# Performance work log

Measured on AMD Instinct MI355X. Metric: run time of the kernel, lower is better.

## Reference

```python
import jax, jax.numpy as jnp
import numpy as np

N = 20000   # nodes
E = 320000  # edges
H = 256     # hidden size == input size (no FeatEncoder branch)


def setup_inputs() -> dict:
    key = jax.random.key(0)
    ks = jax.random.split(key, 10)
    x = jax.random.normal(ks[0], (N, H), dtype=jnp.float32)
    edge_index = jax.random.randint(ks[1], (2, E), 0, N, dtype=jnp.int32)
    s = 1.0 / np.sqrt(H)  # PyG Linear default (glorot-ish uniform)
    inp = {"x": x, "edge_index": edge_index}
    for i, name in enumerate(["W1", "W1_1", "W2", "W3"]):
        inp[name] = jax.random.uniform(ks[2 + i], (H, H), jnp.float32, -s, s)
    for name in ["b1", "b1_1", "b2", "b3"]:
        inp[name] = jnp.zeros((H,), jnp.float32)
    return inp


def gcn_norm(edge_index, num_nodes):
    # add self loops (weight 1.0), symmetric normalization D^-1/2 A D^-1/2
    row, col = edge_index[0], edge_index[1]
    loop = jnp.arange(num_nodes, dtype=row.dtype)
    row = jnp.concatenate([row, loop])
    col = jnp.concatenate([col, loop])
    w = jnp.ones(row.shape[0], dtype=jnp.float32)
    deg = jax.ops.segment_sum(w, col, num_segments=num_nodes)  # in-degree at targets
    dinv = jnp.where(deg > 0, jax.lax.rsqrt(deg), 0.0)
    norm = dinv[row] * dinv[col]  # [E+N]
    return row, col, norm


def conv(x, W, b, row, col, norm, num_nodes):
    # GCNConv: linear transform, gather-scale-scatter-add, bias
    h = x @ W                                   # [N, H]
    msg = norm[:, None] * h[row]                # [E+N, H] gather + scale
    out = jax.ops.segment_sum(msg, col, num_segments=num_nodes)  # scatter-add
    return out + b


def reference(x, edge_index, W1, b1, W1_1, b1_1, W2, b2, W3, b3):
    num_nodes = x.shape[0]
    row, col, norm = gcn_norm(edge_index, num_nodes)
    h1 = jax.nn.relu(conv(x, W1, b1, row, col, norm, num_nodes))
    h2 = jax.nn.relu(conv(h1, W1_1, b1_1, row, col, norm, num_nodes))
    out2 = conv(h2, W2, b2, row, col, norm, num_nodes)
    out3 = conv(h2, W3, b3, row, col, norm, num_nodes)
    return out2, out3
```

## Files before the change

### kernel.cpp

```cpp
#include <hip/hip_runtime.h>
#include <math.h>

#define HD 256

typedef short bf16x8 __attribute__((ext_vector_type(8)));
typedef float f32x4  __attribute__((ext_vector_type(4)));

__device__ __forceinline__ unsigned short f2bf(float f) {
    unsigned u = __builtin_bit_cast(unsigned, f);
    unsigned r = (u + 0x7fffu + ((u >> 16) & 1u)) >> 16;
    return (unsigned short)r;
}
__device__ __forceinline__ float bf2f(unsigned b) {
    return __builtin_bit_cast(float, (b & 0xffffu) << 16);
}



__global__ __launch_bounds__(256) void fillpack_kernel(const int* __restrict__ ei, int E,
                                                       int* __restrict__ cursor,
                                                       int* __restrict__ csr,
                                                       const float* __restrict__ W0,
                                                       const float* __restrict__ W1,
                                                       const float* __restrict__ W2,
                                                       const float* __restrict__ W3,
                                                       unsigned short* __restrict__ pkhi,
                                                       unsigned short* __restrict__ pklo) {
    const int Eb = (E + 255) >> 8;
    const int bid = blockIdx.x;
    if (bid < Eb) {
        int idx = bid * 256 + threadIdx.x;
        if (idx >= E) return;
        int r = ei[idx];
        int c = ei[E + idx];
        int slot = atomicAdd(&cursor[c], 1);
        if (slot < 127) csr[((size_t)c << 7) + slot] = r;
    } else {
        int gid = (bid - Eb) * 256 + threadIdx.x;
        int mat  = gid >> 13;
        int rem  = gid & 8191;
        int nc   = rem >> 9;
        int kc   = (rem >> 6) & 7;
        int lane = rem & 63;
        const float* W = (mat == 0) ? W0 : (mat == 1) ? W1 : (mat == 2) ? W2 : W3;
        int col = nc * 16 + (lane & 15);
        int kb  = kc * 32 + (lane >> 4) * 8;
        alignas(16) unsigned short h[8], l[8];
#pragma unroll
        for (int e = 0; e < 8; ++e) {
            float w = W[(size_t)(kb + e) * HD + col];
            unsigned short hb = f2bf(w);
            h[e] = hb;
            l[e] = f2bf(w - bf2f(hb));
        }
        size_t off = (size_t)mat * 65536 + ((size_t)(nc * 8 + kc) * 64 + lane) * 8;
        *(uint4*)&pkhi[off] = *(const uint4*)h;
        *(uint4*)&pklo[off] = *(const uint4*)l;
    }
}


__global__ __launch_bounds__(256) void finconv_kernel(const int* __restrict__ cursor,
                                                      int* __restrict__ csr,
                                                      const float* __restrict__ x,
                                                      unsigned short* __restrict__ T,
                                                      float* __restrict__ zpad,
                                                      float* __restrict__ tpad,
                                                      int N) {
    const int Fb = (N + 255) >> 8;
    const int Cb = (N * 32 + 255) >> 8;
    const int bid = blockIdx.x;
    if (bid < Fb) {
        int v = bid * 256 + threadIdx.x;
        if (v >= N) return;
        int c = min(cursor[v], 126);
        size_t base = (size_t)v << 7;
        csr[base + c] = v;
        int pad = (c + 8) & ~7;
        for (int s = c + 1; s < pad; ++s) csr[base + s] = N;
    } else if (bid < Fb + Cb) {
        int gid = (bid - Fb) * 256 + threadIdx.x;
        if (gid >= N * 32) return;
        int row = gid >> 5;
        int q   = gid & 31;
        float s = rsqrtf((float)(min(cursor[row], 126) + 1));
        const float4* xp = (const float4*)(x + (size_t)row * HD + q * 8);
        float4 v0 = xp[0], v1 = xp[1];
        float vals[8] = {v0.x, v0.y, v0.z, v0.w, v1.x, v1.y, v1.z, v1.w};
        alignas(16) unsigned short h[8], l[8];
#pragma unroll
        for (int e = 0; e < 8; ++e) {
            float t = vals[e] * s;
            unsigned short hb = f2bf(t);
            h[e] = hb;
            l[e] = f2bf(t - bf2f(hb));
        }
        size_t o = (size_t)row * 512 + (size_t)(q >> 2) * 64 + (q & 3) * 8;
        *(uint4*)&T[o]      = *(const uint4*)h;
        *(uint4*)&T[o + 32] = *(const uint4*)l;
    } else {
        int t = threadIdx.x;
        zpad[t] = 0.f;
        tpad[t] = 0.f;
    }
}


template<int OUTMODE>
__global__ __launch_bounds__(256) void agg_chunk_kernel(const float* __restrict__ zin,
                                                        const int* __restrict__ csr,
                                                        const int* __restrict__ cursor,
                                                        const float* __restrict__ bias,
                                                        void* __restrict__ outBuf, int N) {
    const int chunk = blockIdx.x & 7;
    const int nb    = blockIdx.x >> 3;
    const int wave  = threadIdx.x >> 6;
    const int lane  = threadIdx.x & 63;
    const int slot  = lane & 7;
    const int ni    = lane >> 3;

    int v = nb * 32 + wave * 8 + ni;
    const bool valid = v < N;
    if (!valid) v = N - 1;

    const int cnt  = min(cursor[v], 126) + 1;
    const float dv = rsqrtf((float)cnt);
    const int iters = (cnt + 7) >> 3;
    const int* cp = csr + ((size_t)v << 7);

    const float4* zp = (const float4*)zin;
    const size_t cbase = (size_t)chunk * 8 + slot;

    float a0 = 0.f, a1 = 0.f, a2 = 0.f, a3 = 0.f;
    for (int it = 0; it < iters; ++it) {
        const int* q = cp + it * 8;
        int u0 = q[0], u1 = q[1], u2 = q[2], u3 = q[3];
        int u4 = q[4], u5 = q[5], u6 = q[6], u7 = q[7];
        float4 d0 = zp[(size_t)u0 * 64 + cbase];
        float4 d1 = zp[(size_t)u1 * 64 + cbase];
        float4 d2 = zp[(size_t)u2 * 64 + cbase];
        float4 d3 = zp[(size_t)u3 * 64 + cbase];
        float4 d4 = zp[(size_t)u4 * 64 + cbase];
        float4 d5 = zp[(size_t)u5 * 64 + cbase];
        float4 d6 = zp[(size_t)u6 * 64 + cbase];
        float4 d7 = zp[(size_t)u7 * 64 + cbase];
        a0 += ((d0.x + d1.x) + (d2.x + d3.x)) + ((d4.x + d5.x) + (d6.x + d7.x));
        a1 += ((d0.y + d1.y) + (d2.y + d3.y)) + ((d4.y + d5.y) + (d6.y + d7.y));
        a2 += ((d0.z + d1.z) + (d2.z + d3.z)) + ((d4.z + d5.z) + (d6.z + d7.z));
        a3 += ((d0.w + d1.w) + (d2.w + d3.w)) + ((d4.w + d5.w) + (d6.w + d7.w));
    }
    if (!valid) return;

    float t0, t1, t2, t3;
    if (OUTMODE == 2) {
        t0 = dv * a0; t1 = dv * a1; t2 = dv * a2; t3 = dv * a3;
    } else {
        float4 bv = *(const float4*)&bias[chunk * 32 + slot * 4];
        t0 = dv * fmaxf(fmaf(dv, a0, bv.x), 0.f);
        t1 = dv * fmaxf(fmaf(dv, a1, bv.y), 0.f);
        t2 = dv * fmaxf(fmaf(dv, a2, bv.z), 0.f);
        t3 = dv * fmaxf(fmaf(dv, a3, bv.w), 0.f);
    }

    if (OUTMODE == 1) {
        ((float4*)outBuf)[(size_t)v * 64 + cbase] = make_float4(t0, t1, t2, t3);
    } else {
        unsigned short h0 = f2bf(t0), h1 = f2bf(t1), h2 = f2bf(t2), h3 = f2bf(t3);
        uint2 hw, lw;
        hw.x = h0 | ((unsigned)h1 << 16);
        hw.y = h2 | ((unsigned)h3 << 16);
        unsigned short l0 = f2bf(t0 - bf2f(h0)), l1 = f2bf(t1 - bf2f(h1));
        unsigned short l2 = f2bf(t2 - bf2f(h2)), l3 = f2bf(t3 - bf2f(h3));
        lw.x = l0 | ((unsigned)l1 << 16);
        lw.y = l2 | ((unsigned)l3 << 16);
        unsigned short* T = (unsigned short*)outBuf;
        size_t o = (size_t)v * 512 + chunk * 64 + slot * 4;
        *(uint2*)&T[o]      = hw;
        *(uint2*)&T[o + 32] = lw;
    }
}


template<int NBY>
__global__ __launch_bounds__(256, 3)
void gemm_mfma_kernel(const unsigned short* __restrict__ T,
                      const unsigned short* __restrict__ pkhi,
                      const unsigned short* __restrict__ pklo,
                      const float* __restrict__ ba,
                      const float* __restrict__ bb,
                      float* __restrict__ Ca,
                      float* __restrict__ Cb, int M, int gx) {
    __shared__ unsigned short ldsW[2][2][2048];

    const int id  = blockIdx.x;
    const int xcd = id & 7;
    const int t   = id >> 3;
    const int by  = t & (NBY - 1);
    const int g   = t / NBY;
    const int bx  = xcd + (g << 3);
    if (bx >= gx) return;

    const int tid  = threadIdx.x;
    const int lane = tid & 63;
    const int wave = tid >> 6;

    const int sel = (NBY == 8) ? (by >> 2) : 0;
    const int nc0 = ((NBY == 8) ? (by & 3) : by) * 4;
    const unsigned short* ph = pkhi + (size_t)sel * 65536;
    const unsigned short* pl = pklo + (size_t)sel * 65536;
    float*       C    = sel ? Cb : Ca;
    const float* bias = sel ? bb : ba;

    const int row0  = bx * 128 + wave * 32;
    const int rowA0 = min(row0 + (lane & 15), M - 1);
    const int rowA1 = min(row0 + 16 + (lane & 15), M - 1);
    const int kg    = lane >> 4;

    const unsigned short* aT0 = T + (size_t)rowA0 * 512 + kg * 8;
    const unsigned short* aT1 = T + (size_t)rowA1 * 512 + kg * 8;

    const int snf = tid >> 6;
    const unsigned short* sph = ph + ((size_t)(nc0 + snf) * 8) * 512 + (size_t)(tid & 63) * 8;
    const unsigned short* spl = pl + ((size_t)(nc0 + snf) * 8) * 512 + (size_t)(tid & 63) * 8;

    f32x4 acc[2][4];
#pragma unroll
    for (int f = 0; f < 2; ++f)
#pragma unroll
        for (int j = 0; j < 4; ++j) acc[f][j] = (f32x4)0.f;

    uint4 sh = *(const uint4*)(sph);
    uint4 sl = *(const uint4*)(spl);
    *(uint4*)&ldsW[0][0][tid * 8] = sh;
    *(uint4*)&ldsW[0][1][tid * 8] = sl;
    sh = *(const uint4*)(sph + 512);
    sl = *(const uint4*)(spl + 512);

    bf16x8 a0h[2], a0l[2], a1h[2], a1l[2];
    a0h[0] = *(const bf16x8*)(aT0);
    a0l[0] = *(const bf16x8*)(aT0 + 32);
    a1h[0] = *(const bf16x8*)(aT1);
    a1l[0] = *(const bf16x8*)(aT1 + 32);
    __syncthreads();

#pragma unroll
    for (int kc = 0; kc < 8; ++kc) {
        const int cur = kc & 1;
        if (kc < 7) {
            a0h[cur ^ 1] = *(const bf16x8*)(aT0 + (kc + 1) * 64);
            a0l[cur ^ 1] = *(const bf16x8*)(aT0 + (kc + 1) * 64 + 32);
            a1h[cur ^ 1] = *(const bf16x8*)(aT1 + (kc + 1) * 64);
            a1l[cur ^ 1] = *(const bf16x8*)(aT1 + (kc + 1) * 64 + 32);
        }
        bf16x8 wh[4], wl[4];
#pragma unroll
        for (int j = 0; j < 4; ++j) {
            wh[j] = *(const bf16x8*)&ldsW[cur][0][((size_t)j * 64 + lane) * 8];
            wl[j] = *(const bf16x8*)&ldsW[cur][1][((size_t)j * 64 + lane) * 8];
        }
#pragma unroll
        for (int j = 0; j < 4; ++j) {
            acc[0][j] = __builtin_amdgcn_mfma_f32_16x16x32_bf16(a0h[cur], wh[j], acc[0][j], 0, 0, 0);
            acc[0][j] = __builtin_amdgcn_mfma_f32_16x16x32_bf16(a0h[cur], wl[j], acc[0][j], 0, 0, 0);
            acc[0][j] = __builtin_amdgcn_mfma_f32_16x16x32_bf16(a0l[cur], wh[j], acc[0][j], 0, 0, 0);
            acc[1][j] = __builtin_amdgcn_mfma_f32_16x16x32_bf16(a1h[cur], wh[j], acc[1][j], 0, 0, 0);
            acc[1][j] = __builtin_amdgcn_mfma_f32_16x16x32_bf16(a1h[cur], wl[j], acc[1][j], 0, 0, 0);
            acc[1][j] = __builtin_amdgcn_mfma_f32_16x16x32_bf16(a1l[cur], wh[j], acc[1][j], 0, 0, 0);
        }
        if (kc < 7) {
            *(uint4*)&ldsW[cur ^ 1][0][tid * 8] = sh;
            *(uint4*)&ldsW[cur ^ 1][1][tid * 8] = sl;
            if (kc < 6) {
                sh = *(const uint4*)(sph + (size_t)(kc + 2) * 512);
                sl = *(const uint4*)(spl + (size_t)(kc + 2) * 512);
            }
            __syncthreads();
        }
    }

#pragma unroll
    for (int nf = 0; nf < 4; ++nf) {
        int col = (nc0 + nf) * 16 + (lane & 15);
        float badd = (NBY == 8) ? bias[col] : 0.f;
#pragma unroll
        for (int f = 0; f < 2; ++f) {
#pragma unroll
            for (int r = 0; r < 4; ++r) {
                int row = row0 + f * 16 + kg * 4 + r;
                if (row < M) C[(size_t)row * HD + col] = acc[f][nf][r] + badd;
            }
        }
    }
}


static inline size_t align_up(size_t x, size_t a) { return (x + a - 1) & ~(a - 1); }

extern "C" void kernel_launch(void* const* d_in, const int* in_sizes, int n_in,
                              void* d_out, int out_size, void* d_ws, size_t ws_size,
                              hipStream_t stream) {
    const int N = in_sizes[0] / HD;
    const int E = in_sizes[1] / 2;

    const float* x   = (const float*)d_in[0];
    const int*   ei  = (const int*)d_in[1];
    const float* W1  = (const float*)d_in[2];
    const float* W11 = (const float*)d_in[3];
    const float* W2  = (const float*)d_in[4];
    const float* W3  = (const float*)d_in[5];
    const float* b1  = (const float*)d_in[6];
    const float* b11 = (const float*)d_in[7];
    const float* b2  = (const float*)d_in[8];
    const float* b3  = (const float*)d_in[9];

    float* out2 = (float*)d_out;
    float* out3 = out2 + (size_t)N * HD;

    char* p = (char*)d_ws;
    int*   cursor = (int*)p;   p += align_up((size_t)N * 4, 256);
    int*   csr    = (int*)p;   p += align_up((size_t)N * 128 * 4, 256);
    unsigned short* pkhi = (unsigned short*)p; p += align_up((size_t)4 * 65536 * 2, 256);
    unsigned short* pklo = (unsigned short*)p; p += align_up((size_t)4 * 65536 * 2, 256);
    float* bufZ = (float*)p;   p += align_up((size_t)(N + 1) * HD * 4, 256);
    unsigned short* bufT = (unsigned short*)p; p += align_up((size_t)(N + 1) * 512 * 2, 256);
    (void)ws_size; (void)n_in; (void)out_size;

    const int Eb = (E + 255) / 256;
    const int Fb = (N + 255) / 256;
    const int Cb = (N * 32 + 255) / 256;

    hipMemsetAsync(cursor, 0, (size_t)N * 4, stream);
    fillpack_kernel<<<Eb + 128, 256, 0, stream>>>(ei, E, cursor, csr, W1, W11, W2, W3, pkhi, pklo);
    finconv_kernel<<<Fb + Cb + 1, 256, 0, stream>>>(cursor, csr, x, bufT,
                                                    bufZ + (size_t)N * HD,
                                                    (float*)(bufT + (size_t)N * 512), N);

    const int gx  = (N + 127) / 128;
    const int gxp = ((gx + 7) / 8) * 8;
    const int aggBlocks = 8 * ((N + 31) / 32);

    gemm_mfma_kernel<4><<<gxp * 4, 256, 0, stream>>>(
        bufT, pkhi + 0 * 65536, pklo + 0 * 65536, nullptr, nullptr, bufZ, nullptr, N, gx);
    agg_chunk_kernel<0><<<aggBlocks, 256, 0, stream>>>(bufZ, csr, cursor, b1, bufT, N);

    gemm_mfma_kernel<4><<<gxp * 4, 256, 0, stream>>>(
        bufT, pkhi + 1 * 65536, pklo + 1 * 65536, nullptr, nullptr, bufZ, nullptr, N, gx);
    agg_chunk_kernel<1><<<aggBlocks, 256, 0, stream>>>(bufZ, csr, cursor, b11, bufT, N);

    agg_chunk_kernel<2><<<aggBlocks, 256, 0, stream>>>((const float*)bufT, csr, cursor,
                                                       nullptr, bufZ, N);

    gemm_mfma_kernel<8><<<gxp * 8, 256, 0, stream>>>(
        (const unsigned short*)bufZ, pkhi + 2 * 65536, pklo + 2 * 65536, b2, b3, out2, out3, N, gx);
}
```

Before: 187.9 us.

## Fuse all stages into one persistent cooperative kernel with grid syncs

Replaces the memset and eight separate kernel launches with a single cooperative persistent kernel. Each former kernel becomes a device function executed by grid-stride loops over virtual block ids, with grid.sync() between stages. The aim is to remove launch gaps and per-kernel tail overhead. In exchange the grid is capped to the co-resident block count, which can reduce parallelism and load balance in stages such as the scatter atomics and the GEMMs, and it adds grid-barrier costs.

```diff
diff --git a/kernel.cpp b/kernel.cpp
--- a/kernel.cpp
+++ b/kernel.cpp
@@ -1,5 +1,8 @@
 #include <hip/hip_runtime.h>
+#include <hip/hip_cooperative_groups.h>
 #include <math.h>
+
+namespace cg = cooperative_groups;
 
 #define HD 256
 
@@ -17,26 +20,20 @@
 
 
 
-__global__ __launch_bounds__(256) void fillpack_kernel(const int* __restrict__ ei, int E,
-                                                       int* __restrict__ cursor,
-                                                       int* __restrict__ csr,
-                                                       const float* __restrict__ W0,
-                                                       const float* __restrict__ W1,
-                                                       const float* __restrict__ W2,
-                                                       const float* __restrict__ W3,
-                                                       unsigned short* __restrict__ pkhi,
-                                                       unsigned short* __restrict__ pklo) {
-    const int Eb = (E + 255) >> 8;
-    const int bid = blockIdx.x;
-    if (bid < Eb) {
-        int idx = bid * 256 + threadIdx.x;
+__device__ __forceinline__ void fillpack_body(int vb, int tid, int Eb,
+        const int* __restrict__ ei, int E, int* __restrict__ cursor, int* __restrict__ csr,
+        const float* __restrict__ W0, const float* __restrict__ W1,
+        const float* __restrict__ W2, const float* __restrict__ W3,
+        unsigned short* __restrict__ pkhi, unsigned short* __restrict__ pklo) {
+    if (vb < Eb) {
+        int idx = vb * 256 + tid;
         if (idx >= E) return;
         int r = ei[idx];
         int c = ei[E + idx];
         int slot = atomicAdd(&cursor[c], 1);
         if (slot < 127) csr[((size_t)c << 7) + slot] = r;
     } else {
-        int gid = (bid - Eb) * 256 + threadIdx.x;
+        int gid = (vb - Eb) * 256 + tid;
         int mat  = gid >> 13;
         int rem  = gid & 8191;
         int nc   = rem >> 9;
@@ -59,27 +56,20 @@
     }
 }
 
-
-__global__ __launch_bounds__(256) void finconv_kernel(const int* __restrict__ cursor,
-                                                      int* __restrict__ csr,
-                                                      const float* __restrict__ x,
-                                                      unsigned short* __restrict__ T,
-                                                      float* __restrict__ zpad,
-                                                      float* __restrict__ tpad,
-                                                      int N) {
-    const int Fb = (N + 255) >> 8;
-    const int Cb = (N * 32 + 255) >> 8;
-    const int bid = blockIdx.x;
-    if (bid < Fb) {
-        int v = bid * 256 + threadIdx.x;
+__device__ __forceinline__ void finconv_body(int vb, int tid, int Fb, int Cb,
+        const int* __restrict__ cursor, int* __restrict__ csr,
+        const float* __restrict__ x, unsigned short* __restrict__ T,
+        float* __restrict__ bufZ, int N) {
+    if (vb < Fb) {
+        int v = vb * 256 + tid;
         if (v >= N) return;
         int c = min(cursor[v], 126);
         size_t base = (size_t)v << 7;
         csr[base + c] = v;
         int pad = (c + 8) & ~7;
         for (int s = c + 1; s < pad; ++s) csr[base + s] = N;
-    } else if (bid < Fb + Cb) {
-        int gid = (bid - Fb) * 256 + threadIdx.x;
+    } else if (vb < Fb + Cb) {
+        int gid = (vb - Fb) * 256 + tid;
         if (gid >= N * 32) return;
         int row = gid >> 5;
         int q   = gid & 31;
@@ -99,23 +89,20 @@
         *(uint4*)&T[o]      = *(const uint4*)h;
         *(uint4*)&T[o + 32] = *(const uint4*)l;
     } else {
-        int t = threadIdx.x;
-        zpad[t] = 0.f;
-        tpad[t] = 0.f;
-    }
-}
-
+        bufZ[(size_t)N * HD + tid] = 0.f;
+        ((float*)T)[(size_t)N * HD + tid] = 0.f;
+    }
+}
 
 template<int OUTMODE>
-__global__ __launch_bounds__(256) void agg_chunk_kernel(const float* __restrict__ zin,
-                                                        const int* __restrict__ csr,
-                                                        const int* __restrict__ cursor,
-                                                        const float* __restrict__ bias,
-                                                        void* __restrict__ outBuf, int N) {
-    const int chunk = blockIdx.x & 7;
-    const int nb    = blockIdx.x >> 3;
-    const int wave  = threadIdx.x >> 6;
-    const int lane  = threadIdx.x & 63;
+__device__ __forceinline__ void agg_body(int vb, int tidx,
+        const float* __restrict__ zin, const int* __restrict__ csr,
+        const int* __restrict__ cursor, const float* __restrict__ bias,
+        void* __restrict__ outBuf, int N) {
+    const int chunk = vb & 7;
+    const int nb    = vb >> 3;
+    const int wave  = tidx >> 6;
+    const int lane  = tidx & 63;
     const int slot  = lane & 7;
     const int ni    = lane >> 3;
 
@@ -180,34 +167,26 @@
     }
 }
 
-
 template<int NBY>
-__global__ __launch_bounds__(256, 3)
-void gemm_mfma_kernel(const unsigned short* __restrict__ T,
-                      const unsigned short* __restrict__ pkhi,
-                      const unsigned short* __restrict__ pklo,
-                      const float* __restrict__ ba,
-                      const float* __restrict__ bb,
-                      float* __restrict__ Ca,
-                      float* __restrict__ Cb, int M, int gx) {
-    __shared__ unsigned short ldsW[2][2][2048];
-
-    const int id  = blockIdx.x;
-    const int xcd = id & 7;
-    const int t   = id >> 3;
-    const int by  = t & (NBY - 1);
-    const int g   = t / NBY;
+__device__ __forceinline__ void gemm_body(unsigned short* lds, int vt, int tid,
+        const unsigned short* __restrict__ T,
+        const unsigned short* __restrict__ ph0, const unsigned short* __restrict__ pl0,
+        const float* __restrict__ ba, const float* __restrict__ bb,
+        float* __restrict__ Ca, float* __restrict__ Cb, int M, int gx) {
+    const int xcd = vt & 7;
+    const int tt  = vt >> 3;
+    const int by  = tt & (NBY - 1);
+    const int g   = tt / NBY;
     const int bx  = xcd + (g << 3);
     if (bx >= gx) return;
 
-    const int tid  = threadIdx.x;
     const int lane = tid & 63;
     const int wave = tid >> 6;
 
     const int sel = (NBY == 8) ? (by >> 2) : 0;
     const int nc0 = ((NBY == 8) ? (by & 3) : by) * 4;
-    const unsigned short* ph = pkhi + (size_t)sel * 65536;
-    const unsigned short* pl = pklo + (size_t)sel * 65536;
+    const unsigned short* ph = ph0 + (size_t)sel * 65536;
+    const unsigned short* pl = pl0 + (size_t)sel * 65536;
     float*       C    = sel ? Cb : Ca;
     const float* bias = sel ? bb : ba;
 
@@ -231,8 +210,8 @@
 
     uint4 sh = *(const uint4*)(sph);
     uint4 sl = *(const uint4*)(spl);
-    *(uint4*)&ldsW[0][0][tid * 8] = sh;
-    *(uint4*)&ldsW[0][1][tid * 8] = sl;
+    *(uint4*)&lds[0 * 2048 + tid * 8] = sh;
+    *(uint4*)&lds[1 * 2048 + tid * 8] = sl;
     sh = *(const uint4*)(sph + 512);
     sl = *(const uint4*)(spl + 512);
 
@@ -255,8 +234,8 @@
         bf16x8 wh[4], wl[4];
 #pragma unroll
         for (int j = 0; j < 4; ++j) {
-            wh[j] = *(const bf16x8*)&ldsW[cur][0][((size_t)j * 64 + lane) * 8];
-            wl[j] = *(const bf16x8*)&ldsW[cur][1][((size_t)j * 64 + lane) * 8];
+            wh[j] = *(const bf16x8*)&lds[(cur * 2 + 0) * 2048 + ((size_t)j * 64 + lane) * 8];
+            wl[j] = *(const bf16x8*)&lds[(cur * 2 + 1) * 2048 + ((size_t)j * 64 + lane) * 8];
         }
 #pragma unroll
         for (int j = 0; j < 4; ++j) {
@@ -268,8 +247,8 @@
             acc[1][j] = __builtin_amdgcn_mfma_f32_16x16x32_bf16(a1l[cur], wh[j], acc[1][j], 0, 0, 0);
         }
         if (kc < 7) {
-            *(uint4*)&ldsW[cur ^ 1][0][tid * 8] = sh;
-            *(uint4*)&ldsW[cur ^ 1][1][tid * 8] = sl;
+            *(uint4*)&lds[((cur ^ 1) * 2 + 0) * 2048 + tid * 8] = sh;
+            *(uint4*)&lds[((cur ^ 1) * 2 + 1) * 2048 + tid * 8] = sl;
             if (kc < 6) {
                 sh = *(const uint4*)(sph + (size_t)(kc + 2) * 512);
                 sl = *(const uint4*)(spl + (size_t)(kc + 2) * 512);
@@ -294,13 +273,73 @@
 }
 
 
+__global__ __launch_bounds__(256, 3)
+void mega_kernel(const int* __restrict__ ei, int E, int N,
+                 const float* __restrict__ x,
+                 const float* __restrict__ W1, const float* __restrict__ W11,
+                 const float* __restrict__ W2, const float* __restrict__ W3,
+                 const float* __restrict__ b1, const float* __restrict__ b11,
+                 const float* __restrict__ b2, const float* __restrict__ b3,
+                 int* __restrict__ cursor, int* __restrict__ csr,
+                 unsigned short* __restrict__ pkhi, unsigned short* __restrict__ pklo,
+                 float* __restrict__ bufZ, unsigned short* __restrict__ bufT,
+                 float* __restrict__ out2, float* __restrict__ out3,
+                 int gx, int gxp) {
+    extern __shared__ unsigned short lds[];
+    cg::grid_group grid = cg::this_grid();
+    const int G   = gridDim.x;
+    const int bid = blockIdx.x;
+    const int tid = threadIdx.x;
+
+    const int Eb = (E + 255) >> 8;
+    const int Fb = (N + 255) >> 8;
+    const int Cb = (N * 32 + 255) >> 8;
+    const int aggB = 8 * ((N + 31) / 32);
+
+    for (int i = bid * 256 + tid; i < N; i += G * 256) cursor[i] = 0;
+    grid.sync();
+
+    for (int vb = bid; vb < Eb + 128; vb += G)
+        fillpack_body(vb, tid, Eb, ei, E, cursor, csr, W1, W11, W2, W3, pkhi, pklo);
+    grid.sync();
+
+    for (int vb = bid; vb < Fb + Cb + 1; vb += G)
+        finconv_body(vb, tid, Fb, Cb, cursor, csr, x, bufT, bufZ, N);
+    grid.sync();
+
+    for (int vt = bid; vt < gxp * 4; vt += G)
+        gemm_body<4>(lds, vt, tid, bufT, pkhi, pklo, nullptr, nullptr, bufZ, nullptr, N, gx);
+    grid.sync();
+
+    for (int vb = bid; vb < aggB; vb += G)
+        agg_body<0>(vb, tid, bufZ, csr, cursor, b1, bufT, N);
+    grid.sync();
+
+    for (int vt = bid; vt < gxp * 4; vt += G)
+        gemm_body<4>(lds, vt, tid, bufT, pkhi + 65536, pklo + 65536, nullptr, nullptr, bufZ, nullptr, N, gx);
+    grid.sync();
+
+    for (int vb = bid; vb < aggB; vb += G)
+        agg_body<1>(vb, tid, bufZ, csr, cursor, b11, bufT, N);
+    grid.sync();
+
+    for (int vb = bid; vb < aggB; vb += G)
+        agg_body<2>(vb, tid, (const float*)bufT, csr, cursor, nullptr, bufZ, N);
+    grid.sync();
+
+    for (int vt = bid; vt < gxp * 8; vt += G)
+        gemm_body<8>(lds, vt, tid, (const unsigned short*)bufZ,
+                     pkhi + 2 * 65536, pklo + 2 * 65536, b2, b3, out2, out3, N, gx);
+}
+
+
 static inline size_t align_up(size_t x, size_t a) { return (x + a - 1) & ~(a - 1); }
 
 extern "C" void kernel_launch(void* const* d_in, const int* in_sizes, int n_in,
                               void* d_out, int out_size, void* d_ws, size_t ws_size,
                               hipStream_t stream) {
-    const int N = in_sizes[0] / HD;
-    const int E = in_sizes[1] / 2;
+    int N = in_sizes[0] / HD;
+    int E = in_sizes[1] / 2;
 
     const float* x   = (const float*)d_in[0];
     const int*   ei  = (const int*)d_in[1];
@@ -325,31 +364,26 @@
     unsigned short* bufT = (unsigned short*)p; p += align_up((size_t)(N + 1) * 512 * 2, 256);
     (void)ws_size; (void)n_in; (void)out_size;
 
-    const int Eb = (E + 255) / 256;
-    const int Fb = (N + 255) / 256;
-    const int Cb = (N * 32 + 255) / 256;
-
-    hipMemsetAsync(cursor, 0, (size_t)N * 4, stream);
-    fillpack_kernel<<<Eb + 128, 256, 0, stream>>>(ei, E, cursor, csr, W1, W11, W2, W3, pkhi, pklo);
-    finconv_kernel<<<Fb + Cb + 1, 256, 0, stream>>>(cursor, csr, x, bufT,
-                                                    bufZ + (size_t)N * HD,
-                                                    (float*)(bufT + (size_t)N * 512), N);
-
-    const int gx  = (N + 127) / 128;
-    const int gxp = ((gx + 7) / 8) * 8;
-    const int aggBlocks = 8 * ((N + 31) / 32);
-
-    gemm_mfma_kernel<4><<<gxp * 4, 256, 0, stream>>>(
-        bufT, pkhi + 0 * 65536, pklo + 0 * 65536, nullptr, nullptr, bufZ, nullptr, N, gx);
-    agg_chunk_kernel<0><<<aggBlocks, 256, 0, stream>>>(bufZ, csr, cursor, b1, bufT, N);
-
-    gemm_mfma_kernel<4><<<gxp * 4, 256, 0, stream>>>(
-        bufT, pkhi + 1 * 65536, pklo + 1 * 65536, nullptr, nullptr, bufZ, nullptr, N, gx);
-    agg_chunk_kernel<1><<<aggBlocks, 256, 0, stream>>>(bufZ, csr, cursor, b11, bufT, N);
-
-    agg_chunk_kernel<2><<<aggBlocks, 256, 0, stream>>>((const float*)bufT, csr, cursor,
-                                                       nullptr, bufZ, N);
-
-    gemm_mfma_kernel<8><<<gxp * 8, 256, 0, stream>>>(
-        (const unsigned short*)bufZ, pkhi + 2 * 65536, pklo + 2 * 65536, b2, b3, out2, out3, N, gx);
-}
+    int gx  = (N + 127) / 128;
+    int gxp = ((gx + 7) / 8) * 8;
+
+    int maxbpc = 0;
+    if (hipOccupancyMaxActiveBlocksPerMultiprocessor(&maxbpc, mega_kernel, 256,
+                                                     (size_t)16384) != hipSuccess || maxbpc < 1)
+        maxbpc = 2;
+    int G = maxbpc * 256;
+    if (G > 768) G = 768;
+    G &= ~7;
+    if (G < 64) G = 64;
+
+    void* kargs[] = {
+        (void*)&ei, (void*)&E, (void*)&N, (void*)&x,
+        (void*)&W1, (void*)&W11, (void*)&W2, (void*)&W3,
+        (void*)&b1, (void*)&b11, (void*)&b2, (void*)&b3,
+        (void*)&cursor, (void*)&csr, (void*)&pkhi, (void*)&pklo,
+        (void*)&bufZ, (void*)&bufT, (void*)&out2, (void*)&out3,
+        (void*)&gx, (void*)&gxp
+    };
+    hipLaunchCooperativeKernel((void*)mega_kernel, dim3(G), dim3(256), kargs,
+                               16384u, stream);
+}
```

Result: slower. 689.9 us (+267.1%).
